# Optimization experiments

Measured on AMD Instinct MI355X. Metric: run time of the kernel, lower is better.

## Reference

```python
import jax, jax.numpy as jnp
import numpy as np

NUM_LEVELS = 16
BASE_RES = 16
T = 1 << 19            # hashmap size per level (log2_hashmap_size=19)
LEVEL_DIM = 2
SCALE = 2.0 ** (np.log2(2048.0 / 16.0) / (NUM_LEVELS - 1))  # desired_resolution=2048
PRIME1 = 2654435761
PRIME2 = 805459861
N_POINTS = 524288


def hash_encode(x, tables):
    # x: [N,3] in [0,1]; tables: [NUM_LEVELS, T, LEVEL_DIM]
    x = jnp.clip(x, 0.0, 1.0)
    feats = []
    for l in range(NUM_LEVELS):
        R = int(np.ceil(BASE_RES * SCALE ** l))
        pos = x * R                      # grid has R+1 vertices per axis
        p0f = jnp.floor(pos)
        w = pos - p0f                    # trilinear weights [N,3]
        p0 = p0f.astype(jnp.uint32)
        dense = (R + 1) ** 3 <= T
        acc = jnp.zeros((x.shape[0], LEVEL_DIM), dtype=tables.dtype)
        for c in range(8):               # 8 cube corners
            off = np.array([(c >> d) & 1 for d in range(3)], dtype=np.uint32)
            idx = jnp.minimum(p0 + off[None, :], jnp.uint32(R))
            if dense:
                flat = idx[:, 0] + jnp.uint32(R + 1) * idx[:, 1] + jnp.uint32((R + 1) ** 2) * idx[:, 2]
            else:
                flat = idx[:, 0] ^ (idx[:, 1] * jnp.uint32(PRIME1)) ^ (idx[:, 2] * jnp.uint32(PRIME2))
                flat = flat & jnp.uint32(T - 1)
            wc = jnp.prod(jnp.where(off[None, :] == 1, w, 1.0 - w), axis=-1)
            acc = acc + wc[:, None] * tables[l, flat]
        feats.append(acc)
    return jnp.concatenate(feats, axis=-1)  # [N, 32]


def pos_embed(x):
    # NeRF embedding: include input + sin/cos of 2^0..2^5 * x -> 3 + 36 = 39 dims
    outs = [x]
    for j in range(6):
        f = float(2 ** j)
        outs.append(jnp.sin(f * x))
        outs.append(jnp.cos(f * x))
    return jnp.concatenate(outs, axis=-1)


def wn_linear(h, v, g, b):
    # weight-norm: W = g * v / ||v||_row
    w = g[:, None] * v / jnp.linalg.norm(v, axis=1, keepdims=True)
    return h @ w.T + b


def softplus100(x):
    return jax.nn.softplus(100.0 * x) / 100.0


def setup_inputs() -> dict:
    key = jax.random.key(0)
    ks = jax.random.split(key, 8)
    x = jax.random.uniform(ks[0], (N_POINTS, 3), dtype=jnp.float32)
    tables = jax.random.uniform(ks[1], (NUM_LEVELS, T, LEVEL_DIM), minval=-1e-4, maxval=1e-4, dtype=jnp.float32)
    d_in_mlp = 3 + 36 + NUM_LEVELS * LEVEL_DIM  # 71
    dims = [d_in_mlp, 256, 256, 257]
    params = {}
    for l in range(3):
        fan_out = dims[l + 1]
        v = jax.random.normal(ks[2 + l], (dims[l + 1], dims[l]), dtype=jnp.float32) * np.sqrt(2.0 / fan_out)
        params[f'v{l}'] = v
        params[f'g{l}'] = jnp.linalg.norm(v, axis=1)  # weight_norm init: g = ||v||
        params[f'b{l}'] = jnp.zeros((dims[l + 1],), dtype=jnp.float32)
    return {'x': x, 'tables': tables, **params}


def reference(x, tables, v0, g0, b0, v1, g1, b1, v2, g2, b2):
    # object_center=0, object_scale=1, divide_factor=1 -> encoder sees x directly
    feat = hash_encode(x, tables)
    inp = jnp.concatenate([pos_embed(x), feat], axis=-1)  # [N, 71]
    h = softplus100(wn_linear(inp, v0, g0, b0))
    h = softplus100(wn_linear(h, v1, g1, b1))
    return wn_linear(h, v2, g2, b2)  # [N, 257] = sdf(1) + feature(256)
```

## Files before the change

### kernel.cpp

```cpp
#include <hip/hip_runtime.h>
#include <math.h>

typedef __bf16 bf16;
typedef __attribute__((ext_vector_type(8))) __bf16 bf16x8;
typedef __attribute__((ext_vector_type(4))) float f32x4;
typedef __attribute__((ext_vector_type(4))) short s16x4;

#define T_HASH (1u << 19)
#define PRIME1 2654435761u
#define PRIME2 805459861u
#define FP8_SCALE 8192.0f
#define FP8_INV   (1.0f / 8192.0f)

struct Levels { unsigned R[16]; unsigned mY[16]; unsigned mZ[16]; unsigned df[16]; };

__device__ __forceinline__ unsigned umin_(unsigned a, unsigned b) { return a < b ? a : b; }

__device__ __forceinline__ int swzoff(int row, int colByte) {
    return row * 512 + (colByte ^ ((row & 7) << 4));
}

__device__ __forceinline__ void stb(char* base, int row, int col, float v) {
    *(bf16*)(base + swzoff(row, col * 2)) = (bf16)v;
}
__device__ __forceinline__ void stw(char* base, int row, int col, unsigned short v) {
    *(unsigned short*)(base + swzoff(row, col * 2)) = v;
}

__device__ __forceinline__ float softplus100f(float v) {
    float u = v * 144.2695041f;
    float e = __builtin_amdgcn_exp2f(u);
    float y = __builtin_amdgcn_logf(1.f + e) * 0.006931471806f;
    return v > 0.25f ? v : y;
}

__device__ __forceinline__ unsigned short f2bfu(float v) {
    bf16 h = (bf16)v;
    return *(unsigned short*)&h;
}

__global__ void prep_weights(const float* __restrict__ v0, const float* __restrict__ g0,
                             const float* __restrict__ v1, const float* __restrict__ g1,
                             const float* __restrict__ v2, const float* __restrict__ g2,
                             unsigned short* __restrict__ W0, unsigned short* __restrict__ W1,
                             unsigned short* __restrict__ W2) {
    int r = blockIdx.x;
    int lane = threadIdx.x;
    const float* src = nullptr; const float* g = nullptr; unsigned short* dst; int K, Kp, row;
    if (r < 256)      { row = r;       src = v0 + row * 71;  g = g0; dst = W0 + row * 96;  K = 71;  Kp = 96;  }
    else if (r < 512) { row = r - 256; src = v1 + row * 256; g = g1; dst = W1 + row * 256; K = 256; Kp = 256; }
    else              { row = r - 512; if (row < 257) { src = v2 + row * 256; g = g2; }
                        dst = W2 + row * 256; K = 256; Kp = 256; }
    float ss = 0.f;
    if (src) for (int c = lane; c < K; c += 64) { float v = src[c]; ss += v * v; }
    for (int off = 32; off; off >>= 1) ss += __shfl_down(ss, off);
    ss = __shfl(ss, 0);
    float scale = src ? (g[row] / sqrtf(ss)) : 0.f;
    for (int c = lane; c < Kp; c += 64) {
        float v = (src && c < K) ? src[c] * scale : 0.f;
        dst[c] = f2bfu(v);
    }
}

__global__ void conv_tables(const float2* __restrict__ t, unsigned short* __restrict__ tf8) {
    size_t i = (size_t)blockIdx.x * 256 + threadIdx.x;
    float2 e = t[i];
    int pk = __builtin_amdgcn_cvt_pk_fp8_f32(e.x * FP8_SCALE, e.y * FP8_SCALE, 0, false);
    tf8[i] = (unsigned short)(pk & 0xffff);
}

__global__ __launch_bounds__(256, 8)
void encode_levels(const float* __restrict__ x, const unsigned short* __restrict__ tf8,
                   unsigned* __restrict__ featsLM, Levels lv, int npts) {
    const int slot = blockIdx.x & 7, seq = blockIdx.x >> 3;
    const int l = slot + 8 * (seq & 1);
    const int group = seq >> 1;
    const unsigned Ru = lv.R[l], mY = lv.mY[l], mZ = lv.mZ[l];
    const bool dense = lv.df[l] != 0;
    const unsigned short* __restrict__ tl = tf8 + (size_t)l * T_HASH;
    unsigned* __restrict__ fout = featsLM + (size_t)l * npts;
    const float Rf = (float)Ru;
    const int base = group * 1024 + threadIdx.x;
#pragma unroll
    for (int k = 0; k < 4; ++k) {
        const int p = base + k * 256;
        float xr0 = x[p * 3 + 0], xr1 = x[p * 3 + 1], xr2 = x[p * 3 + 2];
        const float cx = fminf(fmaxf(xr0, 0.f), 1.f);
        const float cy = fminf(fmaxf(xr1, 0.f), 1.f);
        const float cz = fminf(fmaxf(xr2, 0.f), 1.f);
        float px = cx * Rf, py = cy * Rf, pz = cz * Rf;
        float fx = floorf(px), fy = floorf(py), fz = floorf(pz);
        float wx = px - fx, wy = py - fy, wz = pz - fz;
        unsigned ix = (unsigned)fx, iy = (unsigned)fy, iz = (unsigned)fz;
        unsigned xc0 = ix, xc1 = umin_(ix + 1u, Ru);
        unsigned y0 = iy * mY, y1 = umin_(iy + 1u, Ru) * mY;
        unsigned z0 = iz * mZ, z1 = umin_(iz + 1u, Ru) * mZ;
        unsigned yzA[4] = { y0 + z0, y1 + z0, y0 + z1, y1 + z1 };
        float w0x = 1.f - wx, w0y = 1.f - wy, w0z = 1.f - wz;
        float wyz[4] = { w0y * w0z, wy * w0z, w0y * wz, wy * wz };
        float a0 = 0.f, a1 = 0.f;
#pragma unroll
        for (int c = 0; c < 8; ++c) {
            const int ox = c & 1, cyz = c >> 1;
            unsigned xc = ox ? xc1 : xc0;
            unsigned gi = dense ? (xc + yzA[cyz])
                                : ((xc ^ yzA[cyz]) & (T_HASH - 1u));
            unsigned u = (unsigned)tl[gi];
            float ex = __builtin_amdgcn_cvt_f32_fp8(u, 0);
            float ey = __builtin_amdgcn_cvt_f32_fp8(u, 1);
            float wc = (ox ? wx : w0x) * wyz[cyz];
            a0 = fmaf(wc, ex, a0);
            a1 = fmaf(wc, ey, a1);
        }
        a0 *= FP8_INV; a1 *= FP8_INV;
        unsigned outw = (unsigned)f2bfu(a0) | ((unsigned)f2bfu(a1) << 16);
        __builtin_nontemporal_store(outw, &fout[p]);
    }
}


#define STG_STRIDE 260

template<int KSTEPS, int ROWLEN>
__device__ __forceinline__ void layer_mid(const char* __restrict__ inbuf,
                                          const unsigned short* __restrict__ W,
                                          const float* __restrict__ bias,
                                          char* __restrict__ outbuf, int tid) {
    const int lane = tid & 63, wave = tid >> 6;
    const int lrow = lane & 15, lk = lane >> 4;
    const unsigned short* __restrict__ wrow = W + (wave * 16 + lrow) * ROWLEN + lk * 8;
    f32x4 acc[4] = {};
    bf16x8 abuf[3];
    abuf[0] = *(const bf16x8*)(wrow);
    if (KSTEPS > 1) abuf[1] = *(const bf16x8*)(wrow + 32);
#pragma unroll
    for (int ks = 0; ks < KSTEPS; ++ks) {
        if (ks + 2 < KSTEPS) abuf[(ks + 2) % 3] = *(const bf16x8*)(wrow + (ks + 2) * 32);
        const int k0 = ks * 32 + lk * 8;
        bf16x8 b[4];
#pragma unroll
        for (int pt = 0; pt < 4; ++pt)
            b[pt] = *(const bf16x8*)(inbuf + swzoff(pt * 16 + lrow, k0 * 2));
#pragma unroll
        for (int pt = 0; pt < 4; ++pt)
            acc[pt] = __builtin_amdgcn_mfma_f32_16x16x32_bf16(abuf[ks % 3], b[pt], acc[pt], 0, 0, 0);
    }
    const int c0 = wave * 16 + lk * 4;
    const float4 bv = *(const float4*)(bias + c0);
#pragma unroll
    for (int pt = 0; pt < 4; ++pt) {
        const int p = pt * 16 + lrow;
        s16x4 o;
        o.x = (short)f2bfu(softplus100f(acc[pt][0] + bv.x));
        o.y = (short)f2bfu(softplus100f(acc[pt][1] + bv.y));
        o.z = (short)f2bfu(softplus100f(acc[pt][2] + bv.z));
        o.w = (short)f2bfu(softplus100f(acc[pt][3] + bv.w));
        *(s16x4*)(outbuf + swzoff(p, c0 * 2)) = o;
    }
}

__device__ __forceinline__ void layer_fin(const char* __restrict__ inbuf,
                                          const unsigned short* __restrict__ W2,
                                          const float* __restrict__ b2,
                                          float* __restrict__ stg,
                                          float* __restrict__ out, int tid, int blk) {
    const int lane = tid & 63, wave = tid >> 6;
    const int lrow = lane & 15, lk = lane >> 4;
    const unsigned short* __restrict__ wrow = W2 + (wave * 16 + lrow) * 256 + lk * 8;
    f32x4 acc[4] = {};
    bf16x8 abuf[3];
    abuf[0] = *(const bf16x8*)(wrow);
    abuf[1] = *(const bf16x8*)(wrow + 32);
#pragma unroll
    for (int ks = 0; ks < 8; ++ks) {
        if (ks + 2 < 8) abuf[(ks + 2) % 3] = *(const bf16x8*)(wrow + (ks + 2) * 32);
        const int k0 = ks * 32 + lk * 8;
        bf16x8 b[4];
#pragma unroll
        for (int pt = 0; pt < 4; ++pt)
            b[pt] = *(const bf16x8*)(inbuf + swzoff(pt * 16 + lrow, k0 * 2));
#pragma unroll
        for (int pt = 0; pt < 4; ++pt)
            acc[pt] = __builtin_amdgcn_mfma_f32_16x16x32_bf16(abuf[ks % 3], b[pt], acc[pt], 0, 0, 0);
    }
    const int p = tid >> 4, sub = tid & 15;
    float part = 0.f;
    {
        const unsigned short* __restrict__ w2r = W2 + 256 * 256 + sub * 16;
        bf16x8 h0 = *(const bf16x8*)(inbuf + swzoff(p, sub * 32));
        bf16x8 h1 = *(const bf16x8*)(inbuf + swzoff(p, sub * 32 + 16));
        bf16x8 w0 = *(const bf16x8*)(w2r);
        bf16x8 w1 = *(const bf16x8*)(w2r + 8);
#pragma unroll
        for (int j = 0; j < 8; ++j) {
            part = fmaf((float)h0[j], (float)w0[j], part);
            part = fmaf((float)h1[j], (float)w1[j], part);
        }
    }
#pragma unroll
    for (int m = 1; m < 16; m <<= 1) part += __shfl_xor(part, m);

    __syncthreads();
    const int c0 = wave * 16 + lk * 4;
    const float4 bv = *(const float4*)(b2 + c0);
#pragma unroll
    for (int pt = 0; pt < 4; ++pt) {
        const int pr = pt * 16 + lrow;
        f32x4 v;
        v[0] = acc[pt][0] + bv.x;
        v[1] = acc[pt][1] + bv.y;
        v[2] = acc[pt][2] + bv.z;
        v[3] = acc[pt][3] + bv.w;
        *(f32x4*)(stg + pr * STG_STRIDE + c0) = v;
    }
    if (sub == 0) stg[p * STG_STRIDE + 256] = part + b2[256];
    __syncthreads();
    float* __restrict__ dst = out + (size_t)blk * 16448;
#pragma unroll
    for (int r = 0; r < 4; ++r) {
        const int f0 = (r * 1024 + tid) * 4;
        const unsigned pp = ((unsigned)f0 * 65281u) >> 24;
        const int cc = f0 - (int)pp * 257;
        f32x4 v;
#pragma unroll
        for (int u = 0; u < 4; ++u) {
            int c2 = cc + u; unsigned p2 = pp;
            if (c2 >= 257) { c2 -= 257; p2++; }
            v[u] = stg[p2 * STG_STRIDE + c2];
        }
        *(f32x4*)(dst + f0) = v;
    }
    if (tid < 64) {
        const int f0 = 16384 + tid;
        const unsigned pp = ((unsigned)f0 * 65281u) >> 24;
        const int cc = f0 - (int)pp * 257;
        dst[f0] = stg[pp * STG_STRIDE + cc];
    }
}

template<bool SPLIT>
__global__ __launch_bounds__(1024, 8)
void fused_net(const float* __restrict__ x, const float2* __restrict__ tables,
               const unsigned* __restrict__ featsLM,
               const unsigned short* __restrict__ W0, const unsigned short* __restrict__ W1,
               const unsigned short* __restrict__ W2,
               const float* __restrict__ b0, const float* __restrict__ b1, const float* __restrict__ b2,
               float* __restrict__ out, Levels lv, int npts) {
    __shared__ __align__(16) char smem[66560 + 256];
    unsigned* sR  = (unsigned*)(smem + 66560);
    unsigned* sMY = sR + 16;
    unsigned* sMZ = sR + 32;
    unsigned* sDF = sR + 48;
    char* buf0 = smem;
    char* buf1 = smem + 32768;
    float* stg = (float*)smem;
    const int tid = threadIdx.x;
    const int blk = blockIdx.x;

    if (!SPLIT) {
        if (tid >= 960) {
            int i = tid - 960;
            if (i < 16)      sR[i]  = lv.R[i];
            else if (i < 32) sMY[i - 16] = lv.mY[i - 16];
            else if (i < 48) sMZ[i - 32] = lv.mZ[i - 32];
            else             sDF[i - 48] = lv.df[i - 48];
        }
        __syncthreads();
    }

    const int p = tid >> 4, sub = tid & 15;
    const float xr0 = x[(size_t)blk * 192 + p * 3 + 0];
    const float xr1 = x[(size_t)blk * 192 + p * 3 + 1];
    const float xr2 = x[(size_t)blk * 192 + p * 3 + 2];

    if (SPLIT) {
        const int l = tid >> 6, pt = tid & 63;
        unsigned u = featsLM[(size_t)l * npts + blk * 64 + pt];
        stw(buf0, pt, 39 + 2 * l, (unsigned short)(u & 0xffffu));
        stw(buf0, pt, 40 + 2 * l, (unsigned short)(u >> 16));
    }

    if (sub < 13) {
        int c0 = sub * 3;
#pragma unroll
        for (int u = 0; u < 3; ++u) {
            int c = c0 + u;
            if (c >= 39) break;
            float v;
            if (c < 3) v = (c == 0) ? xr0 : (c == 1 ? xr1 : xr2);
            else {
                int q = c - 3, j = q / 6, k = q - j * 6;
                int axis = (k < 3) ? k : k - 3;
                float xv = axis == 0 ? xr0 : (axis == 1 ? xr1 : xr2);
                float fx = (float)(1 << j) * xv;
                v = (k < 3) ? __sinf(fx) : __cosf(fx);
            }
            stb(buf0, p, c, v);
        }
    }
    for (int c = 71 + sub; c < 96; c += 16) stb(buf0, p, c, 0.f);

    if (!SPLIT) {
        const int l = sub;
        const float cx = fminf(fmaxf(xr0, 0.f), 1.f);
        const float cy = fminf(fmaxf(xr1, 0.f), 1.f);
        const float cz = fminf(fmaxf(xr2, 0.f), 1.f);
        const unsigned Ru = sR[l], mY = sMY[l], mZ = sMZ[l];
        const bool dense = sDF[l] != 0;
        const unsigned lofs = (unsigned)l << 19;
        const float Rf = (float)Ru;
        float px = cx * Rf, py = cy * Rf, pz = cz * Rf;
        float fx = floorf(px), fy = floorf(py), fz = floorf(pz);
        float wx = px - fx, wy = py - fy, wz = pz - fz;
        unsigned ix = (unsigned)fx, iy = (unsigned)fy, iz = (unsigned)fz;
        unsigned xc0 = ix, xc1 = umin_(ix + 1u, Ru);
        unsigned y0 = iy * mY, y1 = umin_(iy + 1u, Ru) * mY;
        unsigned z0 = iz * mZ, z1 = umin_(iz + 1u, Ru) * mZ;
        unsigned yzA[4] = { y0 + z0 + lofs, y1 + z0 + lofs, y0 + z1 + lofs, y1 + z1 + lofs };
        unsigned yzX[4] = { y0 ^ z0, y1 ^ z0, y0 ^ z1, y1 ^ z1 };
        float w0x = 1.f - wx, w0y = 1.f - wy, w0z = 1.f - wz;
        float wyz[4] = { w0y * w0z, wy * w0z, w0y * wz, wy * wz };
        float a0 = 0.f, a1 = 0.f;
#pragma unroll
        for (int c = 0; c < 8; ++c) {
            const int ox = c & 1, cyz = c >> 1;
            unsigned xc = ox ? xc1 : xc0;
            unsigned fd = xc + yzA[cyz];
            unsigned fh = ((xc ^ yzX[cyz]) & (T_HASH - 1u)) + lofs;
            unsigned gi = dense ? fd : fh;
            float2 e2 = tables[gi];
            float wc = (ox ? wx : w0x) * wyz[cyz];
            a0 = fmaf(wc, e2.x, a0);
            a1 = fmaf(wc, e2.y, a1);
        }
        stb(buf0, p, 39 + 2 * l, a0);
        stb(buf0, p, 40 + 2 * l, a1);
    }
    __syncthreads();

    layer_mid<3, 96>(buf0, W0, b0, buf1, tid);
    __syncthreads();
    layer_mid<8, 256>(buf1, W1, b1, buf0, tid);
    __syncthreads();
    layer_fin(buf0, W2, b2, stg, out, tid, blk);
}

extern "C" void kernel_launch(void* const* d_in, const int* in_sizes, int n_in,
                              void* d_out, int out_size, void* d_ws, size_t ws_size,
                              hipStream_t stream) {
    const float*  x      = (const float*)d_in[0];
    const float2* tables = (const float2*)d_in[1];
    const float*  v0 = (const float*)d_in[2];
    const float*  g0 = (const float*)d_in[3];
    const float*  b0 = (const float*)d_in[4];
    const float*  v1 = (const float*)d_in[5];
    const float*  g1 = (const float*)d_in[6];
    const float*  b1 = (const float*)d_in[7];
    const float*  v2 = (const float*)d_in[8];
    const float*  g2 = (const float*)d_in[9];
    const float*  b2 = (const float*)d_in[10];

    unsigned short* W0 = (unsigned short*)d_ws;
    unsigned short* W1 = W0 + 256 * 96;
    unsigned short* W2 = W1 + 256 * 256;
    size_t ofs_tf8   = 319488;
    size_t ofs_feats = ofs_tf8 + (size_t)16 * T_HASH * 2;
    size_t need      = ofs_feats + (size_t)16 * T_HASH * 4;
    unsigned short* tf8 = (unsigned short*)((char*)d_ws + ofs_tf8);
    unsigned* featsLM   = (unsigned*)((char*)d_ws + ofs_feats);
    bool use_split = ws_size >= need;

    Levels lv;
    double SCALE = pow(2.0, log2(2048.0 / 16.0) / 15.0);
    for (int l = 0; l < 16; ++l) {
        double r = 16.0 * pow(SCALE, (double)l);
        unsigned R = (unsigned)ceil(r);
        lv.R[l] = R;
        unsigned long long s = (unsigned long long)R + 1;
        int dense = (s * s * s <= (unsigned long long)T_HASH) ? 1 : 0;
        lv.df[l] = dense;
        lv.mY[l] = dense ? (R + 1u) : PRIME1;
        lv.mZ[l] = dense ? (R + 1u) * (R + 1u) : PRIME2;
    }

    prep_weights<<<784, 64, 0, stream>>>(v0, g0, v1, g1, v2, g2, W0, W1, W2);

    int n = in_sizes[0] / 3;
    int nblk = n / 64;

    if (use_split) {
        conv_tables<<<16 * T_HASH / 256, 256, 0, stream>>>(tables, tf8);
        encode_levels<<<8 * (n / 1024) * 2, 256, 0, stream>>>(x, tf8, featsLM, lv, n);
        fused_net<true><<<nblk, 1024, 0, stream>>>(x, tables, featsLM, W0, W1, W2,
                                                   b0, b1, b2, (float*)d_out, lv, n);
    } else {
        fused_net<false><<<nblk, 1024, 0, stream>>>(x, tables, nullptr, W0, W1, W2,
                                                    b0, b1, b2, (float*)d_out, lv, n);
    }
}
```

Measured before the change: 579.7 us.

## Move coarse hash-grid levels from encode kernel into fused MLP kernel

The separate encode_levels kernel now computes only levels 5-15 and writes 11 feature planes instead of 16. The five coarsest (dense, cache-friendly) levels are interpolated inside fused_net from the fp8 tables, by the first five sub-lanes of each point. This cuts the featsLM write and read traffic and the encode kernel's block count. The cost is extra gather and ALU work inside the MLP kernel, an always-on shared-memory setup plus syncthreads, and unbalanced work across sub-lanes.

```diff
diff --git a/kernel.cpp b/kernel.cpp
--- a/kernel.cpp
+++ b/kernel.cpp
@@ -73,12 +73,14 @@
 void encode_levels(const float* __restrict__ x, const unsigned short* __restrict__ tf8,
                    unsigned* __restrict__ featsLM, Levels lv, int npts) {
     const int slot = blockIdx.x & 7, seq = blockIdx.x >> 3;
-    const int l = slot + 8 * (seq & 1);
+    const int round = seq & 1;
+    if (round && slot >= 3) return;
+    const int l = round ? (13 + slot) : (5 + slot);
     const int group = seq >> 1;
     const unsigned Ru = lv.R[l], mY = lv.mY[l], mZ = lv.mZ[l];
     const bool dense = lv.df[l] != 0;
     const unsigned short* __restrict__ tl = tf8 + (size_t)l * T_HASH;
-    unsigned* __restrict__ fout = featsLM + (size_t)l * npts;
+    unsigned* __restrict__ fout = featsLM + (size_t)(l - 5) * npts;
     const float Rf = (float)Ru;
     const int base = group * 1024 + threadIdx.x;
 #pragma unroll
@@ -241,6 +243,7 @@
 template<bool SPLIT>
 __global__ __launch_bounds__(1024, 8)
 void fused_net(const float* __restrict__ x, const float2* __restrict__ tables,
+               const unsigned short* __restrict__ tf8,
                const unsigned* __restrict__ featsLM,
                const unsigned short* __restrict__ W0, const unsigned short* __restrict__ W1,
                const unsigned short* __restrict__ W2,
@@ -257,16 +260,14 @@
     const int tid = threadIdx.x;
     const int blk = blockIdx.x;
 
-    if (!SPLIT) {
-        if (tid >= 960) {
-            int i = tid - 960;
-            if (i < 16)      sR[i]  = lv.R[i];
-            else if (i < 32) sMY[i - 16] = lv.mY[i - 16];
-            else if (i < 48) sMZ[i - 32] = lv.mZ[i - 32];
-            else             sDF[i - 48] = lv.df[i - 48];
-        }
-        __syncthreads();
-    }
+    if (tid >= 960) {
+        int i = tid - 960;
+        if (i < 16)      sR[i]  = lv.R[i];
+        else if (i < 32) sMY[i - 16] = lv.mY[i - 16];
+        else if (i < 48) sMZ[i - 32] = lv.mZ[i - 32];
+        else             sDF[i - 48] = lv.df[i - 48];
+    }
+    __syncthreads();
 
     const int p = tid >> 4, sub = tid & 15;
     const float xr0 = x[(size_t)blk * 192 + p * 3 + 0];
@@ -275,9 +276,11 @@
 
     if (SPLIT) {
         const int l = tid >> 6, pt = tid & 63;
-        unsigned u = featsLM[(size_t)l * npts + blk * 64 + pt];
-        stw(buf0, pt, 39 + 2 * l, (unsigned short)(u & 0xffffu));
-        stw(buf0, pt, 40 + 2 * l, (unsigned short)(u >> 16));
+        if (l < 11) {
+            unsigned u = featsLM[(size_t)l * npts + blk * 64 + pt];
+            stw(buf0, pt, 49 + 2 * l, (unsigned short)(u & 0xffffu));
+            stw(buf0, pt, 50 + 2 * l, (unsigned short)(u >> 16));
+        }
     }
 
     if (sub < 13) {
@@ -300,7 +303,42 @@
     }
     for (int c = 71 + sub; c < 96; c += 16) stb(buf0, p, c, 0.f);
 
-    if (!SPLIT) {
+    if (SPLIT) {
+        if (sub < 5) {
+            const int l = sub;
+            const float cx = fminf(fmaxf(xr0, 0.f), 1.f);
+            const float cy = fminf(fmaxf(xr1, 0.f), 1.f);
+            const float cz = fminf(fmaxf(xr2, 0.f), 1.f);
+            const unsigned Ru = sR[l], mY = sMY[l], mZ = sMZ[l];
+            const unsigned short* __restrict__ tl = tf8 + (size_t)l * T_HASH;
+            const float Rf = (float)Ru;
+            float px = cx * Rf, py = cy * Rf, pz = cz * Rf;
+            float fx = floorf(px), fy = floorf(py), fz = floorf(pz);
+            float wx = px - fx, wy = py - fy, wz = pz - fz;
+            unsigned ix = (unsigned)fx, iy = (unsigned)fy, iz = (unsigned)fz;
+            unsigned xc0 = ix, xc1 = umin_(ix + 1u, Ru);
+            unsigned y0 = iy * mY, y1 = umin_(iy + 1u, Ru) * mY;
+            unsigned z0 = iz * mZ, z1 = umin_(iz + 1u, Ru) * mZ;
+            unsigned yzA[4] = { y0 + z0, y1 + z0, y0 + z1, y1 + z1 };
+            float w0x = 1.f - wx, w0y = 1.f - wy, w0z = 1.f - wz;
+            float wyz[4] = { w0y * w0z, wy * w0z, w0y * wz, wy * wz };
+            float a0 = 0.f, a1 = 0.f;
+#pragma unroll
+            for (int c = 0; c < 8; ++c) {
+                const int ox = c & 1, cyz = c >> 1;
+                unsigned xc = ox ? xc1 : xc0;
+                unsigned gi = xc + yzA[cyz];
+                unsigned u = (unsigned)tl[gi];
+                float ex = __builtin_amdgcn_cvt_f32_fp8(u, 0);
+                float ey = __builtin_amdgcn_cvt_f32_fp8(u, 1);
+                float wc = (ox ? wx : w0x) * wyz[cyz];
+                a0 = fmaf(wc, ex, a0);
+                a1 = fmaf(wc, ey, a1);
+            }
+            stb(buf0, p, 39 + 2 * l, a0 * FP8_INV);
+            stb(buf0, p, 40 + 2 * l, a1 * FP8_INV);
+        }
+    } else {
         const int l = sub;
         const float cx = fminf(fmaxf(xr0, 0.f), 1.f);
         const float cy = fminf(fmaxf(xr1, 0.f), 1.f);
@@ -391,10 +429,10 @@
     if (use_split) {
         conv_tables<<<16 * T_HASH / 256, 256, 0, stream>>>(tables, tf8);
         encode_levels<<<8 * (n / 1024) * 2, 256, 0, stream>>>(x, tf8, featsLM, lv, n);
-        fused_net<true><<<nblk, 1024, 0, stream>>>(x, tables, featsLM, W0, W1, W2,
+        fused_net<true><<<nblk, 1024, 0, stream>>>(x, tables, tf8, featsLM, W0, W1, W2,
                                                    b0, b1, b2, (float*)d_out, lv, n);
     } else {
-        fused_net<false><<<nblk, 1024, 0, stream>>>(x, tables, nullptr, W0, W1, W2,
+        fused_net<false><<<nblk, 1024, 0, stream>>>(x, tables, tf8, nullptr, W0, W1, W2,
                                                     b0, b1, b2, (float*)d_out, lv, n);
     }
 }
```

After: 603.0 us. 4.0% more time.
